# Kernel tuning notes

Hardware: AMD Instinct MI355X
Metric: run time of the kernel (lower is better)

## Reference

```python
import jax, jax.numpy as jnp
import numpy as np

N_NODES = 50000
N_EDGES = 600000
NODE_DIM = 128
EDGE_DIM = 64
HID_DIM = 128
OUT_DIM = 128
BN_EPS = 1e-5


def setup_inputs() -> dict:
    key = jax.random.key(0)
    ks = jax.random.split(key, 16)
    s = 0.02
    return {
        "x": jax.random.normal(ks[0], (N_NODES, NODE_DIM), dtype=jnp.float32),
        "edge_index": jax.random.randint(ks[1], (2, N_EDGES), 0, N_NODES, dtype=jnp.int64),
        "edge_attr": jax.random.normal(ks[2], (N_EDGES, EDGE_DIM), dtype=jnp.float32),
        # conv1 edge lin: edge_dim -> node_dim
        "We1": jax.random.normal(ks[3], (EDGE_DIM, NODE_DIM), dtype=jnp.float32) * s,
        "be1": jnp.zeros((NODE_DIM,), dtype=jnp.float32),
        # conv1 MLP: node_dim -> hid -> hid
        "W1": jax.random.normal(ks[4], (NODE_DIM, HID_DIM), dtype=jnp.float32) * s,
        "b1": jnp.zeros((HID_DIM,), dtype=jnp.float32),
        "W2": jax.random.normal(ks[5], (HID_DIM, HID_DIM), dtype=jnp.float32) * s,
        "b2": jnp.zeros((HID_DIM,), dtype=jnp.float32),
        # conv2 edge lin: edge_dim -> hid
        "We2": jax.random.normal(ks[6], (EDGE_DIM, HID_DIM), dtype=jnp.float32) * s,
        "be2": jnp.zeros((HID_DIM,), dtype=jnp.float32),
        # conv2 MLP: hid -> out -> out
        "W3": jax.random.normal(ks[7], (HID_DIM, OUT_DIM), dtype=jnp.float32) * s,
        "b3": jnp.zeros((OUT_DIM,), dtype=jnp.float32),
        "W4": jax.random.normal(ks[8], (OUT_DIM, OUT_DIM), dtype=jnp.float32) * s,
        "b4": jnp.zeros((OUT_DIM,), dtype=jnp.float32),
        # batch norm affine params
        "gamma": jnp.ones((OUT_DIM,), dtype=jnp.float32),
        "beta": jnp.zeros((OUT_DIM,), dtype=jnp.float32),
    }


def _gine_conv(x, src, dst, edge_attr, We, be, Wa, ba, Wb, bb):
    # message = relu(x_j + Lin(edge_attr)), sum-aggregate at dst, eps = 0
    msg = jax.nn.relu(x[src] + edge_attr @ We + be)          # [E, d]
    aggr = jax.ops.segment_sum(msg, dst, num_segments=x.shape[0])  # [N, d]
    h = x + aggr                                             # (1+eps)*x + aggr
    return jax.nn.relu(h @ Wa + ba) @ Wb + bb


def reference(x, edge_index, edge_attr, We1, be1, W1, b1, W2, b2,
              We2, be2, W3, b3, W4, b4, gamma, beta):
    src, dst = edge_index[0], edge_index[1]
    h = jax.nn.relu(_gine_conv(x, src, dst, edge_attr, We1, be1, W1, b1, W2, b2))
    h = _gine_conv(h, src, dst, edge_attr, We2, be2, W3, b3, W4, b4)
    # BatchNorm1d (training mode: batch statistics, biased variance)
    mean = jnp.mean(h, axis=0)
    var = jnp.mean(jnp.square(h - mean), axis=0)
    return gamma * (h - mean) * jax.lax.rsqrt(var + BN_EPS) + beta
```

## Files before the change

kernel.cpp:

```cpp
#include <hip/hip_runtime.h>

#define NDIM 128
#define EDIM 64
#define BN_EPS 1e-5f
#define SPAN 64
#define WPB  4
#define LPAD (NDIM + 4)
#define PITCH 136

typedef __attribute__((ext_vector_type(8))) short short8v;
typedef __attribute__((ext_vector_type(4))) float float4v;

static __device__ __forceinline__ unsigned short f2bf(float f) {
    union { float f; unsigned u; } c; c.f = f;
    const unsigned r = (c.u + 0x7fffu + ((c.u >> 16) & 1u)) >> 16;
    return (unsigned short)r;
}

static __device__ __forceinline__ short8v pack_bf(const float4 f0, const float4 f1) {
    short8v a;
    a[0] = (short)f2bf(f0.x); a[1] = (short)f2bf(f0.y);
    a[2] = (short)f2bf(f0.z); a[3] = (short)f2bf(f0.w);
    a[4] = (short)f2bf(f1.x); a[5] = (short)f2bf(f1.y);
    a[6] = (short)f2bf(f1.z); a[7] = (short)f2bf(f1.w);
    return a;
}

static __device__ __forceinline__ short8v cvt_row(const float* __restrict__ arow, int k0) {
    const float4 f0 = *reinterpret_cast<const float4*>(arow + k0);
    const float4 f1 = *reinterpret_cast<const float4*>(arow + k0 + 4);
    return pack_bf(f0, f1);
}

__global__ __launch_bounds__(256) void hist_k(
    const int* __restrict__ ei, int* __restrict__ deg, int E)
{
    const int e = blockIdx.x * blockDim.x + threadIdx.x;
    if (e < E) atomicAdd(&deg[ei[E + e]], 1);
}

__global__ __launch_bounds__(1024) void scan_build(
    int* __restrict__ cursor, int* __restrict__ rowptr, int N)
{
    __shared__ int wsums[16];
    __shared__ int run_s;
    const int tid  = threadIdx.x;
    const int lane = tid & 63;
    const int w    = tid >> 6;
    if (tid == 0) run_s = 0;
    __syncthreads();
    for (int base = 0; base < N; base += 1024) {
        const int i = base + tid;
        const int v = (i < N) ? cursor[i] : 0;
        int incl = v;
#pragma unroll
        for (int off = 1; off < 64; off <<= 1) {
            int t = __shfl_up(incl, off, 64);
            if (lane >= off) incl += t;
        }
        if (lane == 63) wsums[w] = incl;
        __syncthreads();
        if (w == 0) {
            int s = (lane < 16) ? wsums[lane] : 0;
#pragma unroll
            for (int off = 1; off < 16; off <<= 1) {
                int t = __shfl_up(s, off, 64);
                if (lane >= off) s += t;
            }
            if (lane < 16) wsums[lane] = s;
        }
        __syncthreads();
        const int waveoff = (w > 0) ? wsums[w - 1] : 0;
        const int run = run_s;
        const int excl = run + waveoff + incl - v;
        if (i < N) { rowptr[i] = excl; cursor[i] = excl; }
        __syncthreads();
        if (tid == 0) run_s += wsums[15];
        __syncthreads();
    }
    if (tid == 0) rowptr[N] = run_s;
}

__global__ __launch_bounds__(256) void scatter_k(
    const int* __restrict__ ei, int* __restrict__ cursor,
    int* __restrict__ srcp, int* __restrict__ eidp, int* __restrict__ dstp, int E)
{
    const int e = blockIdx.x * blockDim.x + threadIdx.x;
    if (e < E) {
        const int d = ei[E + e];
        const int p = atomicAdd(&cursor[d], 1);
        srcp[p] = ei[e];
        eidp[p] = e;
        dstp[p] = d;
    }
}

__global__ __launch_bounds__(128) void prep_all(
    const float* __restrict__ We1, const float* __restrict__ We2,
    const float* __restrict__ W1, const float* __restrict__ W2,
    const float* __restrict__ W3, const float* __restrict__ W4,
    unsigned short* __restrict__ WeT1, unsigned short* __restrict__ WeT2,
    unsigned short* __restrict__ W1T, unsigned short* __restrict__ W2T,
    unsigned short* __restrict__ W3T, unsigned short* __restrict__ W4T)
{
    const int c = blockIdx.x;
    const int k = threadIdx.x;
    if (k < EDIM) {
        WeT1[c * EDIM + k] = f2bf(We1[k * NDIM + c]);
        WeT2[c * EDIM + k] = f2bf(We2[k * NDIM + c]);
    }
    W1T[c * NDIM + k] = f2bf(W1[k * NDIM + c]);
    W2T[c * NDIM + k] = f2bf(W2[k * NDIM + c]);
    W3T[c * NDIM + k] = f2bf(W3[k * NDIM + c]);
    W4T[c * NDIM + k] = f2bf(W4[k * NDIM + c]);
}

__global__ __launch_bounds__(256) void edge_mfma(
    const float* __restrict__ xnode,
    const float* __restrict__ ea,
    const int*   __restrict__ srcp,
    const int*   __restrict__ eidp,
    const int*   __restrict__ dstp,
    const unsigned short* __restrict__ WeT,
    const float* __restrict__ be,
    float*       __restrict__ aggr,
    int E)
{
    __shared__ float msg[WPB][16][LPAD];

    const int tid   = threadIdx.x;
    const int lane  = tid & 63;
    const int wv    = tid >> 6;
    const int span0 = (blockIdx.x * WPB + wv) * SPAN;
    if (span0 >= E) return;

    const int m16 = lane & 15;
    const int kg  = lane >> 4;
    const int k0a = kg * 8;

    short8v bfrag[2][8];
#pragma unroll
    for (int kk = 0; kk < 2; ++kk)
#pragma unroll
        for (int nt = 0; nt < 8; ++nt) {
            const int col = nt * 16 + m16;
            bfrag[kk][nt] = *reinterpret_cast<const short8v*>(&WeT[col * EDIM + kk * 32 + k0a]);
        }

    const int c0 = lane, c1 = lane + 64;
    const float be0 = be[c0], be1 = be[c1];
    float* msgw = &msg[wv][0][0];

    float a0 = 0.f, a1 = 0.f;

    if (span0 + SPAN <= E) {
        int   sr_c[16], ds_c[16];
        float xv0_c[16], xv1_c[16];
        float4 eaf_n[4];
        float4 eaf_nn[4];

#pragma unroll
        for (int s = 0; s < 16; ++s) { sr_c[s] = srcp[span0 + s]; ds_c[s] = dstp[span0 + s]; }
#pragma unroll
        for (int s = 0; s < 16; ++s) {
            xv0_c[s] = xnode[(long)sr_c[s] * NDIM + c0];
            xv1_c[s] = xnode[(long)sr_c[s] * NDIM + c1];
        }
        {
            const float* arow = ea + (long)eidp[span0 + m16] * EDIM;
            short8v af0 = cvt_row(arow, k0a);
            short8v af1 = cvt_row(arow, 32 + k0a);
#pragma unroll
            for (int nt = 0; nt < 8; ++nt) {
                float4v acc = (float4v){0.f, 0.f, 0.f, 0.f};
                acc = __builtin_amdgcn_mfma_f32_16x16x32_bf16(af0, bfrag[0][nt], acc, 0, 0, 0);
                acc = __builtin_amdgcn_mfma_f32_16x16x32_bf16(af1, bfrag[1][nt], acc, 0, 0, 0);
#pragma unroll
                for (int r = 0; r < 4; ++r)
                    msgw[(kg * 4 + r) * LPAD + nt * 16 + m16] = acc[r];
            }
        }
        {
            const float* arow = ea + (long)eidp[span0 + 16 + m16] * EDIM;
            eaf_n[0] = *reinterpret_cast<const float4*>(arow + k0a);
            eaf_n[1] = *reinterpret_cast<const float4*>(arow + k0a + 4);
            eaf_n[2] = *reinterpret_cast<const float4*>(arow + 32 + k0a);
            eaf_n[3] = *reinterpret_cast<const float4*>(arow + 32 + k0a + 4);
        }

        int dcur = ds_c[0];

#pragma unroll
        for (int t = 0; t < SPAN / 16; ++t) {
            const int base = span0 + t * 16;
            const bool hn  = (t + 1 < SPAN / 16);
            const bool hnn = (t + 2 < SPAN / 16);
            int   sr_n[16], ds_n[16];
            float xv0_n[16], xv1_n[16];

            if (hn) {
#pragma unroll
                for (int s = 0; s < 16; ++s) {
                    sr_n[s] = srcp[base + 16 + s];
                    ds_n[s] = dstp[base + 16 + s];
                }
#pragma unroll
                for (int s = 0; s < 16; ++s) {
                    xv0_n[s] = xnode[(long)sr_n[s] * NDIM + c0];
                    xv1_n[s] = xnode[(long)sr_n[s] * NDIM + c1];
                }
            }

            if (hnn) {
                const float* arow = ea + (long)eidp[base + 32 + m16] * EDIM;
                eaf_nn[0] = *reinterpret_cast<const float4*>(arow + k0a);
                eaf_nn[1] = *reinterpret_cast<const float4*>(arow + k0a + 4);
                eaf_nn[2] = *reinterpret_cast<const float4*>(arow + 32 + k0a);
                eaf_nn[3] = *reinterpret_cast<const float4*>(arow + 32 + k0a + 4);
            }

#pragma unroll
            for (int s = 0; s < 16; ++s) {
                if (ds_c[s] != dcur) {
                    atomicAdd(&aggr[(long)dcur * NDIM + c0], a0);
                    atomicAdd(&aggr[(long)dcur * NDIM + c1], a1);
                    a0 = 0.f; a1 = 0.f; dcur = ds_c[s];
                }
                a0 += fmaxf(xv0_c[s] + msgw[s * LPAD + c0] + be0, 0.f);
                a1 += fmaxf(xv1_c[s] + msgw[s * LPAD + c1] + be1, 0.f);
            }

            if (hn) {
                const short8v af0 = pack_bf(eaf_n[0], eaf_n[1]);
                const short8v af1 = pack_bf(eaf_n[2], eaf_n[3]);
#pragma unroll
                for (int nt = 0; nt < 8; ++nt) {
                    float4v acc = (float4v){0.f, 0.f, 0.f, 0.f};
                    acc = __builtin_amdgcn_mfma_f32_16x16x32_bf16(af0, bfrag[0][nt], acc, 0, 0, 0);
                    acc = __builtin_amdgcn_mfma_f32_16x16x32_bf16(af1, bfrag[1][nt], acc, 0, 0, 0);
#pragma unroll
                    for (int r = 0; r < 4; ++r)
                        msgw[(kg * 4 + r) * LPAD + nt * 16 + m16] = acc[r];
                }
#pragma unroll
                for (int i = 0; i < 4; ++i) eaf_n[i] = eaf_nn[i];
#pragma unroll
                for (int s = 0; s < 16; ++s) {
                    sr_c[s] = sr_n[s]; ds_c[s] = ds_n[s];
                    xv0_c[s] = xv0_n[s]; xv1_c[s] = xv1_n[s];
                }
            }
        }
        atomicAdd(&aggr[(long)dcur * NDIM + c0], a0);
        atomicAdd(&aggr[(long)dcur * NDIM + c1], a1);
    } else {
        const int spanEnd = E;
        int dcur = dstp[span0];
        for (int t = 0; t < SPAN / 16; ++t) {
            const int base = span0 + t * 16;
            if (base >= spanEnd) break;

            const int  slot = (base + m16 < E) ? base + m16 : E - 1;
            const float* arow = ea + (long)eidp[slot] * EDIM;
            short8v afrag[2];
            afrag[0] = cvt_row(arow, k0a);
            afrag[1] = cvt_row(arow, 32 + k0a);

#pragma unroll
            for (int nt = 0; nt < 8; ++nt) {
                float4v acc = (float4v){0.f, 0.f, 0.f, 0.f};
                acc = __builtin_amdgcn_mfma_f32_16x16x32_bf16(afrag[0], bfrag[0][nt], acc, 0, 0, 0);
                acc = __builtin_amdgcn_mfma_f32_16x16x32_bf16(afrag[1], bfrag[1][nt], acc, 0, 0, 0);
#pragma unroll
                for (int r = 0; r < 4; ++r)
                    msgw[(kg * 4 + r) * LPAD + nt * 16 + m16] = acc[r];
            }

            for (int s = 0; s < 16; ++s) {
                const int gs = base + s;
                if (gs >= spanEnd) break;
                const int d  = dstp[gs];
                const int sr = srcp[gs];
                if (d != dcur) {
                    atomicAdd(&aggr[(long)dcur * NDIM + c0], a0);
                    atomicAdd(&aggr[(long)dcur * NDIM + c1], a1);
                    a0 = 0.f; a1 = 0.f; dcur = d;
                }
                const float xv0 = xnode[(long)sr * NDIM + c0];
                const float xv1 = xnode[(long)sr * NDIM + c1];
                a0 += fmaxf(xv0 + msgw[s * LPAD + c0] + be0, 0.f);
                a1 += fmaxf(xv1 + msgw[s * LPAD + c1] + be1, 0.f);
            }
        }
        atomicAdd(&aggr[(long)dcur * NDIM + c0], a0);
        atomicAdd(&aggr[(long)dcur * NDIM + c1], a1);
    }
}

template <bool FINAL_RELU, bool STATS>
__global__ __launch_bounds__(256) void node_mlp_mfma(
    const float* xin,
    const float* __restrict__ aggr,
    const unsigned short* __restrict__ W1T, const float* __restrict__ b1,
    const unsigned short* __restrict__ W2T, const float* __restrict__ b2,
    float* out,
    float* __restrict__ stats,
    int N)
{
    __shared__ unsigned short in_lds[16][PITCH];
    __shared__ unsigned short t_lds[16][PITCH];

    const int tid  = threadIdx.x;
    const int lane = tid & 63;
    const int wv   = tid >> 6;
    const int wn0  = wv * 32;
    const int m16  = lane & 15;
    const int rg   = lane >> 4;

    short8v b1f[4][2], b2f[4][2];
#pragma unroll
    for (int kt = 0; kt < 4; ++kt)
#pragma unroll
        for (int nt = 0; nt < 2; ++nt) {
            const int col = wn0 + nt * 16 + m16;
            b1f[kt][nt] = *reinterpret_cast<const short8v*>(&W1T[col * NDIM + kt * 32 + rg * 8]);
            b2f[kt][nt] = *reinterpret_cast<const short8v*>(&W2T[col * NDIM + kt * 32 + rg * 8]);
        }
    float bias1[2], bias2[2];
#pragma unroll
    for (int nt = 0; nt < 2; ++nt) {
        bias1[nt] = b1[wn0 + nt * 16 + m16];
        bias2[nt] = b2[wn0 + nt * 16 + m16];
    }

    float ss[2] = {0.f, 0.f}, sq[2] = {0.f, 0.f};

    const int ntile = (N + 15) >> 4;
    for (int tile = blockIdx.x; tile < ntile; tile += gridDim.x) {
        const int nb = tile << 4;

        {
            const int row = tid >> 4;
            const int ch  = tid & 15;
            const int gr  = nb + row;
            short8v pk = (short8v){0, 0, 0, 0, 0, 0, 0, 0};
            if (gr < N) {
                const float4* xp = reinterpret_cast<const float4*>(xin  + (size_t)gr * NDIM + ch * 8);
                const float4* ap = reinterpret_cast<const float4*>(aggr + (size_t)gr * NDIM + ch * 8);
                const float4 x0 = xp[0], x1 = xp[1];
                const float4 g0 = ap[0], g1 = ap[1];
                pk[0] = (short)f2bf(x0.x + g0.x); pk[1] = (short)f2bf(x0.y + g0.y);
                pk[2] = (short)f2bf(x0.z + g0.z); pk[3] = (short)f2bf(x0.w + g0.w);
                pk[4] = (short)f2bf(x1.x + g1.x); pk[5] = (short)f2bf(x1.y + g1.y);
                pk[6] = (short)f2bf(x1.z + g1.z); pk[7] = (short)f2bf(x1.w + g1.w);
            }
            *reinterpret_cast<short8v*>(&in_lds[row][ch * 8]) = pk;
        }
        __syncthreads();

        short8v af[4];
#pragma unroll
        for (int kt = 0; kt < 4; ++kt)
            af[kt] = *reinterpret_cast<const short8v*>(&in_lds[m16][kt * 32 + rg * 8]);
        float4v acc[2];
#pragma unroll
        for (int nt = 0; nt < 2; ++nt) {
            acc[nt] = (float4v){0.f, 0.f, 0.f, 0.f};
#pragma unroll
            for (int kt = 0; kt < 4; ++kt)
                acc[nt] = __builtin_amdgcn_mfma_f32_16x16x32_bf16(af[kt], b1f[kt][nt], acc[nt], 0, 0, 0);
        }
#pragma unroll
        for (int nt = 0; nt < 2; ++nt)
#pragma unroll
            for (int r = 0; r < 4; ++r) {
                const float v = fmaxf(acc[nt][r] + bias1[nt], 0.f);
                t_lds[rg * 4 + r][wn0 + nt * 16 + m16] = f2bf(v);
            }
        __syncthreads();

#pragma unroll
        for (int kt = 0; kt < 4; ++kt)
            af[kt] = *reinterpret_cast<const short8v*>(&t_lds[m16][kt * 32 + rg * 8]);
        float4v acc2[2];
#pragma unroll
        for (int nt = 0; nt < 2; ++nt) {
            acc2[nt] = (float4v){0.f, 0.f, 0.f, 0.f};
#pragma unroll
            for (int kt = 0; kt < 4; ++kt)
                acc2[nt] = __builtin_amdgcn_mfma_f32_16x16x32_bf16(af[kt], b2f[kt][nt], acc2[nt], 0, 0, 0);
        }

#pragma unroll
        for (int nt = 0; nt < 2; ++nt)
#pragma unroll
            for (int r = 0; r < 4; ++r) {
                const int node = nb + rg * 4 + r;
                if (node < N) {
                    float o = acc2[nt][r] + bias2[nt];
                    if (FINAL_RELU) o = fmaxf(o, 0.f);
                    out[(size_t)node * NDIM + wn0 + nt * 16 + m16] = o;
                    if (STATS) { ss[nt] += o; sq[nt] += o * o; }
                }
            }
    }

    if (STATS) {
#pragma unroll
        for (int nt = 0; nt < 2; ++nt) {
            float s = ss[nt], q = sq[nt];
            s += __shfl_xor(s, 16); q += __shfl_xor(q, 16);
            s += __shfl_xor(s, 32); q += __shfl_xor(q, 32);
            if (rg == 0) {
                atomicAdd(&stats[wn0 + nt * 16 + m16], s);
                atomicAdd(&stats[NDIM + wn0 + nt * 16 + m16], q);
            }
        }
    }
}

__global__ __launch_bounds__(256) void bn_apply(
    float* out,
    const float* __restrict__ stats,
    const float* __restrict__ gamma,
    const float* __restrict__ beta,
    int N)
{
    __shared__ float sc_s[NDIM];
    __shared__ float sh_s[NDIM];
    const float invN = 1.f / (float)N;
    if (threadIdx.x < NDIM) {
        const int f = threadIdx.x;
        const float mean = stats[f] * invN;
        const float var  = stats[NDIM + f] * invN - mean * mean;
        const float sc   = gamma[f] * rsqrtf(var + BN_EPS);
        sc_s[f] = sc;
        sh_s[f] = beta[f] - mean * sc;
    }
    __syncthreads();

    const int total4 = N * (NDIM / 4);
    float4* o4 = reinterpret_cast<float4*>(out);
    for (int idx = blockIdx.x * blockDim.x + threadIdx.x; idx < total4;
         idx += gridDim.x * blockDim.x) {
        const int fb = (idx & 31) * 4;
        float4 p = o4[idx];
        p.x = p.x * sc_s[fb + 0] + sh_s[fb + 0];
        p.y = p.y * sc_s[fb + 1] + sh_s[fb + 1];
        p.z = p.z * sc_s[fb + 2] + sh_s[fb + 2];
        p.w = p.w * sc_s[fb + 3] + sh_s[fb + 3];
        o4[idx] = p;
    }
}

extern "C" void kernel_launch(void* const* d_in, const int* in_sizes, int n_in,
                              void* d_out, int out_size, void* d_ws, size_t ws_size,
                              hipStream_t stream)
{
    const float* x    = (const float*)d_in[0];
    const int*   ei   = (const int*)  d_in[1];
    const float* ea   = (const float*)d_in[2];
    const float* We1  = (const float*)d_in[3];
    const float* be1  = (const float*)d_in[4];
    const float* W1   = (const float*)d_in[5];
    const float* b1   = (const float*)d_in[6];
    const float* W2   = (const float*)d_in[7];
    const float* b2   = (const float*)d_in[8];
    const float* We2  = (const float*)d_in[9];
    const float* be2  = (const float*)d_in[10];
    const float* W3   = (const float*)d_in[11];
    const float* b3   = (const float*)d_in[12];
    const float* W4   = (const float*)d_in[13];
    const float* b4   = (const float*)d_in[14];
    const float* gamma = (const float*)d_in[15];
    const float* beta  = (const float*)d_in[16];

    const int N = in_sizes[0] / NDIM;
    const int E = in_sizes[1] / 2;

    float*          aggr   = (float*)d_ws;
    unsigned short* WeT1   = (unsigned short*)(aggr + (size_t)N * NDIM);
    unsigned short* WeT2   = WeT1 + NDIM * EDIM;
    unsigned short* W1T    = WeT2 + NDIM * EDIM;
    unsigned short* W2T    = W1T + NDIM * NDIM;
    unsigned short* W3T    = W2T + NDIM * NDIM;
    unsigned short* W4T    = W3T + NDIM * NDIM;
    int*            rowptr = (int*)(W4T + NDIM * NDIM);
    int*            cursor = rowptr + (N + 1);
    int*            srcp   = cursor + N;
    int*            eidp   = srcp + E;
    int*            dstp   = eidp + E;
    float*          stats  = (float*)(dstp + E);
    float*          h      = (float*)d_out;

    hipMemsetAsync(cursor, 0, (size_t)N * sizeof(int), stream);
    hipMemsetAsync(stats, 0, 2 * NDIM * sizeof(float), stream);

    hist_k<<<(E + 255) / 256, 256, 0, stream>>>(ei, cursor, E);
    scan_build<<<1, 1024, 0, stream>>>(cursor, rowptr, N);
    scatter_k<<<(E + 255) / 256, 256, 0, stream>>>(ei, cursor, srcp, eidp, dstp, E);
    prep_all<<<NDIM, NDIM, 0, stream>>>(We1, We2, W1, W2, W3, W4,
                                        WeT1, WeT2, W1T, W2T, W3T, W4T);

    const int egrid = (E + WPB * SPAN - 1) / (WPB * SPAN);
    const int mgrid = 625;

    hipMemsetAsync(aggr, 0, (size_t)N * NDIM * sizeof(float), stream);
    edge_mfma<<<egrid, 256, 0, stream>>>(x, ea, srcp, eidp, dstp, WeT1, be1, aggr, E);
    node_mlp_mfma<true, false><<<mgrid, 256, 0, stream>>>(x, aggr, W1T, b1, W2T, b2,
                                                          h, nullptr, N);
    hipMemsetAsync(aggr, 0, (size_t)N * NDIM * sizeof(float), stream);
    edge_mfma<<<egrid, 256, 0, stream>>>(h, ea, srcp, eidp, dstp, WeT2, be2, aggr, E);
    node_mlp_mfma<false, true><<<mgrid, 256, 0, stream>>>(h, aggr, W3T, b3, W4T, b4,
                                                          h, stats, N);
    bn_apply<<<1024, 256, 0, stream>>>(h, stats, gamma, beta, N);
}
```

Measured before the change: 444.1 us.

## Pre-permute edge attributes into dst-sorted bf16 layout for edge kernels

Adds a permute_ea kernel that converts edge_attr to bf16 once and writes it in dst-sorted (CSR) order, using a new slotof map filled in by scatter_k. Both edge_mfma passes then read contiguous bf16 rows instead of gathering fp32 rows through eidp and converting them. This halves the bytes read and makes the edge-attribute loads coalesced in two passes, at the cost of one extra full read and write of edge_attr. The path is used only when the workspace is large enough, and otherwise falls back to the old code.

```diff
diff --git a/kernel.cpp b/kernel.cpp
--- a/kernel.cpp
+++ b/kernel.cpp
@@ -9,6 +9,7 @@
 #define PITCH 136
 
 typedef __attribute__((ext_vector_type(8))) short short8v;
+typedef __attribute__((ext_vector_type(4))) short short4v;
 typedef __attribute__((ext_vector_type(4))) float float4v;
 
 static __device__ __forceinline__ unsigned short f2bf(float f) {
@@ -83,15 +84,40 @@
 
 __global__ __launch_bounds__(256) void scatter_k(
     const int* __restrict__ ei, int* __restrict__ cursor,
-    int* __restrict__ srcp, int* __restrict__ eidp, int* __restrict__ dstp, int E)
+    int* __restrict__ srcp, int* __restrict__ dstp,
+    int* __restrict__ slotof, int* __restrict__ eidp, int E)
 {
     const int e = blockIdx.x * blockDim.x + threadIdx.x;
     if (e < E) {
         const int d = ei[E + e];
         const int p = atomicAdd(&cursor[d], 1);
-        srcp[p] = ei[e];
-        eidp[p] = e;
-        dstp[p] = d;
+        srcp[p]   = ei[e];
+        dstp[p]   = d;
+        slotof[e] = p;
+        eidp[p]   = e;
+    }
+}
+
+__global__ __launch_bounds__(256) void permute_ea(
+    const float* __restrict__ ea, const int* __restrict__ slotof,
+    unsigned short* __restrict__ eap, int E)
+{
+    const int tid  = threadIdx.x;
+    const int lane = tid & 63;
+    const int wv   = tid >> 6;
+    const int q    = lane >> 4;
+    const int j    = lane & 15;
+    const int nw   = gridDim.x * 4;
+    for (int g = blockIdx.x * 4 + wv; g * 4 < E; g += nw) {
+        const int e = g * 4 + q;
+        if (e < E) {
+            const float4 v = *reinterpret_cast<const float4*>(ea + (size_t)e * EDIM + j * 4);
+            short4v pk;
+            pk[0] = (short)f2bf(v.x); pk[1] = (short)f2bf(v.y);
+            pk[2] = (short)f2bf(v.z); pk[3] = (short)f2bf(v.w);
+            const int sl = slotof[e];
+            *reinterpret_cast<short4v*>(eap + (size_t)sl * EDIM + j * 4) = pk;
+        }
     }
 }
 
@@ -115,9 +141,11 @@
     W4T[c * NDIM + k] = f2bf(W4[k * NDIM + c]);
 }
 
+template <bool PERM>
 __global__ __launch_bounds__(256) void edge_mfma(
     const float* __restrict__ xnode,
     const float* __restrict__ ea,
+    const unsigned short* __restrict__ eap,
     const int*   __restrict__ srcp,
     const int*   __restrict__ eidp,
     const int*   __restrict__ dstp,
@@ -156,6 +184,8 @@
     if (span0 + SPAN <= E) {
         int   sr_c[16], ds_c[16];
         float xv0_c[16], xv1_c[16];
+        short8v af_n[2];
+        short8v af_nn[2];
         float4 eaf_n[4];
         float4 eaf_nn[4];
 
@@ -167,9 +197,16 @@
             xv1_c[s] = xnode[(long)sr_c[s] * NDIM + c1];
         }
         {
-            const float* arow = ea + (long)eidp[span0 + m16] * EDIM;
-            short8v af0 = cvt_row(arow, k0a);
-            short8v af1 = cvt_row(arow, 32 + k0a);
+            short8v af0, af1;
+            if (PERM) {
+                const unsigned short* arow = eap + (size_t)(span0 + m16) * EDIM;
+                af0 = *reinterpret_cast<const short8v*>(arow + k0a);
+                af1 = *reinterpret_cast<const short8v*>(arow + 32 + k0a);
+            } else {
+                const float* arow = ea + (long)eidp[span0 + m16] * EDIM;
+                af0 = cvt_row(arow, k0a);
+                af1 = cvt_row(arow, 32 + k0a);
+            }
 #pragma unroll
             for (int nt = 0; nt < 8; ++nt) {
                 float4v acc = (float4v){0.f, 0.f, 0.f, 0.f};
@@ -180,7 +217,11 @@
                     msgw[(kg * 4 + r) * LPAD + nt * 16 + m16] = acc[r];
             }
         }
-        {
+        if (PERM) {
+            const unsigned short* arow = eap + (size_t)(span0 + 16 + m16) * EDIM;
+            af_n[0] = *reinterpret_cast<const short8v*>(arow + k0a);
+            af_n[1] = *reinterpret_cast<const short8v*>(arow + 32 + k0a);
+        } else {
             const float* arow = ea + (long)eidp[span0 + 16 + m16] * EDIM;
             eaf_n[0] = *reinterpret_cast<const float4*>(arow + k0a);
             eaf_n[1] = *reinterpret_cast<const float4*>(arow + k0a + 4);
@@ -212,11 +253,17 @@
             }
 
             if (hnn) {
-                const float* arow = ea + (long)eidp[base + 32 + m16] * EDIM;
-                eaf_nn[0] = *reinterpret_cast<const float4*>(arow + k0a);
-                eaf_nn[1] = *reinterpret_cast<const float4*>(arow + k0a + 4);
-                eaf_nn[2] = *reinterpret_cast<const float4*>(arow + 32 + k0a);
-                eaf_nn[3] = *reinterpret_cast<const float4*>(arow + 32 + k0a + 4);
+                if (PERM) {
+                    const unsigned short* arow = eap + (size_t)(base + 32 + m16) * EDIM;
+                    af_nn[0] = *reinterpret_cast<const short8v*>(arow + k0a);
+                    af_nn[1] = *reinterpret_cast<const short8v*>(arow + 32 + k0a);
+                } else {
+                    const float* arow = ea + (long)eidp[base + 32 + m16] * EDIM;
+                    eaf_nn[0] = *reinterpret_cast<const float4*>(arow + k0a);
+                    eaf_nn[1] = *reinterpret_cast<const float4*>(arow + k0a + 4);
+                    eaf_nn[2] = *reinterpret_cast<const float4*>(arow + 32 + k0a);
+                    eaf_nn[3] = *reinterpret_cast<const float4*>(arow + 32 + k0a + 4);
+                }
             }
 
 #pragma unroll
@@ -231,8 +278,9 @@
             }
 
             if (hn) {
-                const short8v af0 = pack_bf(eaf_n[0], eaf_n[1]);
-                const short8v af1 = pack_bf(eaf_n[2], eaf_n[3]);
+                short8v af0, af1;
+                if (PERM) { af0 = af_n[0]; af1 = af_n[1]; }
+                else      { af0 = pack_bf(eaf_n[0], eaf_n[1]); af1 = pack_bf(eaf_n[2], eaf_n[3]); }
 #pragma unroll
                 for (int nt = 0; nt < 8; ++nt) {
                     float4v acc = (float4v){0.f, 0.f, 0.f, 0.f};
@@ -242,8 +290,12 @@
                     for (int r = 0; r < 4; ++r)
                         msgw[(kg * 4 + r) * LPAD + nt * 16 + m16] = acc[r];
                 }
-#pragma unroll
-                for (int i = 0; i < 4; ++i) eaf_n[i] = eaf_nn[i];
+                if (PERM) {
+                    af_n[0] = af_nn[0]; af_n[1] = af_nn[1];
+                } else {
+#pragma unroll
+                    for (int i = 0; i < 4; ++i) eaf_n[i] = eaf_nn[i];
+                }
 #pragma unroll
                 for (int s = 0; s < 16; ++s) {
                     sr_c[s] = sr_n[s]; ds_c[s] = ds_n[s];
@@ -260,11 +312,17 @@
             const int base = span0 + t * 16;
             if (base >= spanEnd) break;
 
-            const int  slot = (base + m16 < E) ? base + m16 : E - 1;
-            const float* arow = ea + (long)eidp[slot] * EDIM;
+            const int slot = (base + m16 < E) ? base + m16 : E - 1;
             short8v afrag[2];
-            afrag[0] = cvt_row(arow, k0a);
-            afrag[1] = cvt_row(arow, 32 + k0a);
+            if (PERM) {
+                const unsigned short* arow = eap + (size_t)slot * EDIM;
+                afrag[0] = *reinterpret_cast<const short8v*>(arow + k0a);
+                afrag[1] = *reinterpret_cast<const short8v*>(arow + 32 + k0a);
+            } else {
+                const float* arow = ea + (long)eidp[slot] * EDIM;
+                afrag[0] = cvt_row(arow, k0a);
+                afrag[1] = cvt_row(arow, 32 + k0a);
+            }
 
 #pragma unroll
             for (int nt = 0; nt < 8; ++nt) {
@@ -488,29 +546,42 @@
     int*            rowptr = (int*)(W4T + NDIM * NDIM);
     int*            cursor = rowptr + (N + 1);
     int*            srcp   = cursor + N;
-    int*            eidp   = srcp + E;
-    int*            dstp   = eidp + E;
-    float*          stats  = (float*)(dstp + E);
-    float*          h      = (float*)d_out;
+    int*            dstp   = srcp + E;
+    int*            slotof = dstp + E;
+    int*            eidp   = slotof + E;
+    float*          stats  = (float*)(eidp + E);
+    unsigned short* eap    = (unsigned short*)(stats + 2 * NDIM);
+
+    const size_t need_perm = (size_t)((char*)eap - (char*)d_ws) + (size_t)E * EDIM * 2 + 64;
+    const bool   perm      = ws_size >= need_perm;
 
     hipMemsetAsync(cursor, 0, (size_t)N * sizeof(int), stream);
     hipMemsetAsync(stats, 0, 2 * NDIM * sizeof(float), stream);
 
     hist_k<<<(E + 255) / 256, 256, 0, stream>>>(ei, cursor, E);
     scan_build<<<1, 1024, 0, stream>>>(cursor, rowptr, N);
-    scatter_k<<<(E + 255) / 256, 256, 0, stream>>>(ei, cursor, srcp, eidp, dstp, E);
+    scatter_k<<<(E + 255) / 256, 256, 0, stream>>>(ei, cursor, srcp, dstp, slotof, eidp, E);
     prep_all<<<NDIM, NDIM, 0, stream>>>(We1, We2, W1, W2, W3, W4,
                                         WeT1, WeT2, W1T, W2T, W3T, W4T);
+    if (perm)
+        permute_ea<<<1024, 256, 0, stream>>>(ea, slotof, eap, E);
 
     const int egrid = (E + WPB * SPAN - 1) / (WPB * SPAN);
     const int mgrid = 625;
+    float* h = (float*)d_out;
 
     hipMemsetAsync(aggr, 0, (size_t)N * NDIM * sizeof(float), stream);
-    edge_mfma<<<egrid, 256, 0, stream>>>(x, ea, srcp, eidp, dstp, WeT1, be1, aggr, E);
+    if (perm)
+        edge_mfma<true><<<egrid, 256, 0, stream>>>(x, ea, eap, srcp, eidp, dstp, WeT1, be1, aggr, E);
+    else
+        edge_mfma<false><<<egrid, 256, 0, stream>>>(x, ea, eap, srcp, eidp, dstp, WeT1, be1, aggr, E);
     node_mlp_mfma<true, false><<<mgrid, 256, 0, stream>>>(x, aggr, W1T, b1, W2T, b2,
                                                           h, nullptr, N);
     hipMemsetAsync(aggr, 0, (size_t)N * NDIM * sizeof(float), stream);
-    edge_mfma<<<egrid, 256, 0, stream>>>(h, ea, srcp, eidp, dstp, WeT2, be2, aggr, E);
+    if (perm)
+        edge_mfma<true><<<egrid, 256, 0, stream>>>(h, ea, eap, srcp, eidp, dstp, WeT2, be2, aggr, E);
+    else
+        edge_mfma<false><<<egrid, 256, 0, stream>>>(h, ea, eap, srcp, eidp, dstp, WeT2, be2, aggr, E);
     node_mlp_mfma<false, true><<<mgrid, 256, 0, stream>>>(h, aggr, W3T, b3, W4T, b4,
                                                           h, stats, N);
     bn_apply<<<1024, 256, 0, stream>>>(h, stats, gamma, beta, N);
```

New measurement: 422.3 us. -4.9%, faster.
